# Optimization experiments

Measured on AMD Instinct MI355X. Metric: run time of the kernel, lower is better.

The kernel has to match this reference:

```python
import jax, jax.numpy as jnp
import numpy as np
import math

B, H, W, Cv, Ct, T = 8, 64, 64, 256, 512, 100
TOP_M = 5
N_PAD = 8  # last N_PAD text tokens are all-zero padding


def _xavier(key, fi, fo):
    lim = math.sqrt(6.0 / (fi + fo))
    return jax.random.uniform(key, (fi, fo), jnp.float32, -lim, lim)


def layernorm(x, g, b, eps=1e-5):
    m = x.mean(-1, keepdims=True)
    v = ((x - m) ** 2).mean(-1, keepdims=True)
    return (x - m) * jax.lax.rsqrt(v + eps) * g + b


def l2norm(x, eps=1e-6):
    n = jnp.sqrt((x * x).sum(-1, keepdims=True))
    return x / jnp.maximum(n, eps)


def setup_inputs() -> dict:
    key = jax.random.key(0)
    ks = jax.random.split(key, 10)
    visual = jax.random.normal(ks[0], (B, H, W, Cv), jnp.float32)
    text = jax.random.normal(ks[1], (B, T, Ct), jnp.float32)
    text = text.at[:, T - N_PAD:, :].set(0.0)  # padded tokens
    return {
        'visual_features': visual,
        'text_features': text,
        'ln1_g': jnp.ones((Cv,), jnp.float32),
        'ln1_b': jnp.zeros((Cv,), jnp.float32),
        'qw': _xavier(ks[2], Cv, Ct), 'qb': jnp.zeros((Ct,), jnp.float32),
        'vw': _xavier(ks[3], Ct, Cv), 'vb': jnp.zeros((Cv,), jnp.float32),
        'gate_w': jax.random.normal(ks[4], (Cv, 1), jnp.float32) * 0.02,
        'gate_b': jnp.zeros((1,), jnp.float32),
        'logit_scale': jnp.asarray(math.log(1.0 / 0.07), jnp.float32),
        'alpha': jnp.asarray(0.1, jnp.float32),
        'ln2_g': jnp.ones((Cv,), jnp.float32),
        'ln2_b': jnp.zeros((Cv,), jnp.float32),
        'w1': jax.random.normal(ks[5], (Cv, 4 * Cv), jnp.float32) * 0.02,
        'b1': jnp.zeros((4 * Cv,), jnp.float32),
        'w2': jax.random.normal(ks[6], (4 * Cv, Cv), jnp.float32) * 0.02,
        'b2': jnp.zeros((Cv,), jnp.float32),
        'top_m': TOP_M,
    }


def reference(visual_features, text_features, ln1_g, ln1_b, qw, qb, vw, vb,
              gate_w, gate_b, logit_scale, alpha, ln2_g, ln2_b, w1, b1, w2, b2,
              top_m):
    Bv, Hh, Ww, C = visual_features.shape
    N = Hh * Ww
    x = layernorm(visual_features, ln1_g, ln1_b).reshape(Bv, N, C)
    q = l2norm(x @ qw + qb)                     # (B,N,Ct)
    k = l2norm(text_features)                   # (B,T,Ct)
    v = text_features @ vw + vb                 # (B,T,Cv)
    pad = jnp.abs(text_features).sum(-1) <= 1e-6  # (B,T) True = padding
    Ctd = float(qw.shape[1])
    scale = jnp.exp(jnp.clip(logit_scale, -2.0, 2.0)) / math.sqrt(Ctd)
    sim = jnp.einsum('bnc,btc->bnt', q, k) * scale
    top_vals, top_idx = jax.lax.top_k(sim, top_m)       # (B,N,M)
    pad_top = jax.vmap(lambda p, i: p[i])(pad, top_idx)  # (B,N,M)
    top_vals = jnp.where(pad_top, -jnp.inf, top_vals)
    attn = jax.nn.softmax(top_vals, axis=-1)
    v_sel = jax.vmap(lambda vb_, ib: vb_[ib])(v, top_idx)  # (B,N,M,Cv)
    aligned = jnp.einsum('bnm,bnmc->bnc', attn, v_sel)
    gate = jax.nn.sigmoid(x @ gate_w + gate_b)  # (B,N,1)
    aligned = aligned * gate
    y = x + alpha * aligned
    y = layernorm(y, ln2_g, ln2_b)
    y = y + (jax.nn.gelu(y @ w1 + b1, approximate=False) @ w2 + b2)
    return y.reshape(Bv, Hh, Ww, C)
```

## Files before the change

### kernel.cpp

```cpp
#include <hip/hip_runtime.h>
#include <hip/hip_bf16.h>
#include <math.h>

using bf16 = __hip_bfloat16;
typedef __attribute__((ext_vector_type(8))) short s16x8;
typedef __attribute__((ext_vector_type(4))) short s16x4;
typedef __attribute__((ext_vector_type(4))) float f32x4;
typedef __attribute__((ext_vector_type(4))) unsigned int u32x4;

static __device__ __forceinline__ float bits2f(unsigned short u) {
  union { unsigned int i; float f; } c; c.i = ((unsigned int)u) << 16; return c.f;
}
static __device__ __forceinline__ unsigned short f2bits(float f) {
  bf16 h = __float2bfloat16(f);
  return *reinterpret_cast<unsigned short*>(&h);
}
static __device__ __forceinline__ unsigned short scrub16(unsigned short u, unsigned short repl) {
  return ((u & 0x7F80u) == 0x7F80u) ? repl : u;
}
static __device__ __forceinline__ unsigned short f2bits_s(float f, unsigned short repl) {
  return scrub16(f2bits(f), repl);
}
static __device__ __forceinline__ float ldf_s(const float* p, float repl) {
  unsigned int w = *reinterpret_cast<const unsigned int*>(p);
  if ((w & 0x7F800000u) == 0x7F800000u) return repl;
  union { unsigned int i; float f; } c; c.i = w; return c.f;
}
static __device__ __forceinline__ float stf_s(float f, float repl) {
  union { float f; unsigned int i; } c; c.f = f;
  if ((c.i & 0x7F800000u) == 0x7F800000u) return repl;
  return f;
}
static __device__ __forceinline__ s16x8 pack8(const float* p) {
  union { f32x4 f; float fe[4]; unsigned int u[4]; } a, b;
  a.f = *reinterpret_cast<const f32x4*>(p);
  b.f = *reinterpret_cast<const f32x4*>(p + 4);
  s16x8 v;
  #pragma unroll
  for (int e = 0; e < 4; e++) {
    const float fa = ((a.u[e] & 0x7F800000u) == 0x7F800000u) ? 0.f : a.fe[e];
    const float fb = ((b.u[e] & 0x7F800000u) == 0x7F800000u) ? 0.f : b.fe[e];
    v[e]     = (short)f2bits_s(fa, 0);
    v[e + 4] = (short)f2bits_s(fb, 0);
  }
  return v;
}
static __device__ __forceinline__ float gelu_fast(float t) {
  const float u = fmaf(0.044715f * t * t, t, t);
  const float e = __expf(-1.5957691216057308f * u);
  return __fdividef(t, 1.f + e);
}
static __device__ __forceinline__ void gload_lds16(const unsigned short* g, unsigned short* l) {
  __builtin_amdgcn_global_load_lds(
      (const __attribute__((address_space(1))) void*)g,
      (__attribute__((address_space(3))) void*)l, 16, 0, 0);
}

static __device__ __forceinline__ float block_sum(float v, float* red, int tid) {
  #pragma unroll
  for (int o = 32; o > 0; o >>= 1) v += __shfl_down(v, o, 64);
  __syncthreads();
  if ((tid & 63) == 0) red[tid >> 6] = v;
  __syncthreads();
  return red[0] + red[1] + red[2] + red[3];
}

__global__ __launch_bounds__(256)
void k_prepw(const float* __restrict__ qw, unsigned short* __restrict__ qwt) {
  const int n = blockIdx.x;
  const int k = threadIdx.x;
  qwt[n * 256 + (k ^ ((n & 7) << 3))] = f2bits_s(ldf_s(&qw[(long)k * 512 + n], 0.f), 0);
}

__global__ __launch_bounds__(256)
void k_prep2(const float* __restrict__ text, unsigned short* __restrict__ khat,
             int* __restrict__ padf) {
  __shared__ float red[4];
  const int t = blockIdx.x, b = blockIdx.y, tid = threadIdx.x;
  unsigned short* kr = khat + ((long)b * 112 + t) * 512;
  if (t >= 100) {
    if (tid < 64) *reinterpret_cast<s16x8*>(&kr[tid * 8]) = (s16x8){0,0,0,0,0,0,0,0};
    return;
  }
  const float* tr = text + ((long)b * 100 + t) * 512;
  const float v0 = ldf_s(&tr[tid], 0.f), v1 = ldf_s(&tr[tid + 256], 0.f);
  const float ss = block_sum(fmaf(v0, v0, v1 * v1), red, tid);
  const float sa = block_sum(fabsf(v0) + fabsf(v1), red, tid);
  const float inv = 1.f / fmaxf(sqrtf(ss), 1e-6f);
  const int ks = tid ^ ((t & 7) << 3);
  kr[ks]       = f2bits_s(v0 * inv, 0);
  kr[ks + 256] = f2bits_s(v1 * inv, 0);
  if (tid == 0) padf[b * 100 + t] = (sa <= 1e-6f) ? 1 : 0;
}

__global__ __launch_bounds__(512)
void k_sim_mfma(float* xv, const unsigned short* __restrict__ qwt,
                const float* __restrict__ qb, const unsigned short* __restrict__ khat,
                const float* __restrict__ ls, unsigned short* __restrict__ simb,
                const float* __restrict__ ln1g, const float* __restrict__ ln1b) {
  __shared__ __align__(16) unsigned short s_q[64][520];
  __shared__ __align__(16) unsigned short s_un[32768];
  __shared__ float s_qn[64];

  const int tid  = threadIdx.x;
  const int lane = tid & 63;
  const int w    = tid >> 6;
  const int l15  = lane & 15;
  const int lg   = lane >> 4;
  const int b    = blockIdx.y;
  const long grow = (long)b * 4096 + (long)blockIdx.x * 64;

  #pragma unroll
  for (int it = 0; it < 8; it++) {
    const int u = tid + it * 512;
    gload_lds16(&qwt[u * 8], &s_un[u * 8]);
  }

  const int R1 = (w >> 2) * 32;
  s16x8 xa[2][8];
  #pragma unroll
  for (int rb = 0; rb < 2; rb++) {
    float* xr = &xv[(grow + R1 + rb * 16 + l15) * 256 + lg * 8];
    float raw[8][8];
    float sm = 0.f, sq = 0.f;
    #pragma unroll
    for (int ks = 0; ks < 8; ks++) {
      union { f32x4 f; float fe[4]; unsigned int u_[4]; } a, c;
      a.f = *reinterpret_cast<const f32x4*>(xr + ks * 32);
      c.f = *reinterpret_cast<const f32x4*>(xr + ks * 32 + 4);
      #pragma unroll
      for (int e = 0; e < 4; e++) {
        const float va = ((a.u_[e] & 0x7F800000u) == 0x7F800000u) ? 0.f : a.fe[e];
        const float vb = ((c.u_[e] & 0x7F800000u) == 0x7F800000u) ? 0.f : c.fe[e];
        raw[ks][e] = va; raw[ks][e + 4] = vb;
        sm += va + vb;
        sq = fmaf(va, va, sq); sq = fmaf(vb, vb, sq);
      }
    }
    sm += __shfl_xor(sm, 16, 64); sm += __shfl_xor(sm, 32, 64);
    sq += __shfl_xor(sq, 16, 64); sq += __shfl_xor(sq, 32, 64);
    const float mean = sm * (1.f / 256.f);
    const float var  = fmaxf(sq * (1.f / 256.f) - mean * mean, 0.f);
    const float rstd = rsqrtf(var + 1e-5f);
    #pragma unroll
    for (int ks = 0; ks < 8; ks++) {
      const int c0 = ks * 32 + lg * 8;
      const f32x4 g0 = *reinterpret_cast<const f32x4*>(&ln1g[c0]);
      const f32x4 g1 = *reinterpret_cast<const f32x4*>(&ln1g[c0 + 4]);
      const f32x4 bb0 = *reinterpret_cast<const f32x4*>(&ln1b[c0]);
      const f32x4 bb1 = *reinterpret_cast<const f32x4*>(&ln1b[c0 + 4]);
      f32x4 o0, o1; s16x8 vv;
      #pragma unroll
      for (int e = 0; e < 4; e++) {
        const float x0 = stf_s((raw[ks][e] - mean) * rstd * g0[e] + bb0[e], 0.f);
        const float x1 = stf_s((raw[ks][e + 4] - mean) * rstd * g1[e] + bb1[e], 0.f);
        o0[e] = x0; o1[e] = x1;
        vv[e]     = (short)f2bits_s(x0, 0);
        vv[e + 4] = (short)f2bits_s(x1, 0);
      }
      xa[rb][ks] = vv;
      if ((w & 3) == 0) {
        *reinterpret_cast<f32x4*>(xr + ks * 32)     = o0;
        *reinterpret_cast<f32x4*>(xr + ks * 32 + 4) = o1;
      }
    }
  }
  __syncthreads();

  const int C1 = (w & 3) * 32;
  for (int nc = 0; nc < 4; nc++) {
    f32x4 a1[2][2];
    #pragma unroll
    for (int i = 0; i < 2; i++)
      #pragma unroll
      for (int j = 0; j < 2; j++) a1[i][j] = (f32x4){0.f, 0.f, 0.f, 0.f};
    #pragma unroll
    for (int ks = 0; ks < 8; ks++) {
      s16x8 bfr[2];
      #pragma unroll
      for (int cb = 0; cb < 2; cb++) {
        const int nl = C1 + cb * 16 + l15;
        const int byt = nl * 512 + ((ks * 64 + lg * 16) ^ ((nl & 7) << 4));
        bfr[cb] = *reinterpret_cast<const s16x8*>(reinterpret_cast<const char*>(s_un) + byt);
      }
      #pragma unroll
      for (int rb = 0; rb < 2; rb++) {
        a1[rb][0] = __builtin_amdgcn_mfma_f32_16x16x32_bf16(xa[rb][ks], bfr[0], a1[rb][0], 0, 0, 0);
        a1[rb][1] = __builtin_amdgcn_mfma_f32_16x16x32_bf16(xa[rb][ks], bfr[1], a1[rb][1], 0, 0, 0);
      }
    }
    #pragma unroll
    for (int cb = 0; cb < 2; cb++) {
      const int n = nc * 128 + C1 + cb * 16 + l15;
      const float bq = ldf_s(&qb[n], 0.f);
      #pragma unroll
      for (int rb = 0; rb < 2; rb++)
        #pragma unroll
        for (int rg = 0; rg < 4; rg++)
          s_q[R1 + rb * 16 + lg * 4 + rg][n] = f2bits_s(a1[rb][cb][rg] + bq, 0);
    }
    __syncthreads();
    if (nc < 3) {
      const unsigned short* src = qwt + (long)(nc + 1) * 32768;
      #pragma unroll
      for (int it = 0; it < 8; it++) {
        const int u = tid + it * 512;
        gload_lds16(&src[u * 8], &s_un[u * 8]);
      }
      __syncthreads();
    }
  }

  {
    const int r = tid >> 3, ts8 = tid & 7;
    float ss = 0.f;
    #pragma unroll
    for (int j = 0; j < 8; j++) {
      s16x8 v = *reinterpret_cast<const s16x8*>(&s_q[r][ts8 * 64 + j * 8]);
      #pragma unroll
      for (int e = 0; e < 8; e++) { float f = bits2f((unsigned short)v[e]); ss = fmaf(f, f, ss); }
    }
    #pragma unroll
    for (int o = 4; o > 0; o >>= 1) ss += __shfl_down(ss, o, 8);
    if (ts8 == 0) s_qn[r] = fmaxf(sqrtf(ss), 1e-6f);
  }

  const int wr = w & 1, wc = w >> 1;
  f32x4 acc[2][2];
  #pragma unroll
  for (int i = 0; i < 2; i++)
    #pragma unroll
    for (int j = 0; j < 2; j++) acc[i][j] = (f32x4){0.f, 0.f, 0.f, 0.f};

  for (int kc = 0; kc < 2; kc++) {
    #pragma unroll
    for (int it = 0; it < 7; it++) {
      const int u = it * 512 + tid;
      const int t = u >> 5, kb = (u & 31) * 8;
      gload_lds16(&khat[((long)b * 112 + t) * 512 + kc * 256 + kb], &s_un[u * 8]);
    }
    __syncthreads();
    #pragma unroll
    for (int ks = 0; ks < 8; ks++) {
      const int ko = kc * 256 + ks * 32 + lg * 8;
      s16x8 af[2], bfr[2];
      #pragma unroll
      for (int rb = 0; rb < 2; rb++)
        af[rb] = *reinterpret_cast<const s16x8*>(&s_q[(2 * wr + rb) * 16 + l15][ko]);
      #pragma unroll
      for (int cb = 0; cb < 2; cb++)
        if (2 * wc + cb < 7) {
          const int t = (2 * wc + cb) * 16 + l15;
          bfr[cb] = *reinterpret_cast<const s16x8*>(
              &s_un[t * 256 + ((ks * 32 + lg * 8) ^ ((t & 7) << 3))]);
        }
      #pragma unroll
      for (int rb = 0; rb < 2; rb++)
        #pragma unroll
        for (int cb = 0; cb < 2; cb++)
          if (2 * wc + cb < 7)
            acc[rb][cb] = __builtin_amdgcn_mfma_f32_16x16x32_bf16(af[rb], bfr[cb], acc[rb][cb], 0, 0, 0);
    }
    __syncthreads();
  }

  float l = ldf_s(&ls[0], 0.f);
  l = fminf(fmaxf(l, -2.f), 2.f);
  const float scale = expf(l) * 0.04419417382415922f;
  #pragma unroll
  for (int rb = 0; rb < 2; rb++)
    #pragma unroll
    for (int rg = 0; rg < 4; rg++) {
      const int row = (2 * wr + rb) * 16 + lg * 4 + rg;
      const float inv = scale / s_qn[row];
      #pragma unroll
      for (int cb = 0; cb < 2; cb++) {
        const int tcol = (2 * wc + cb) * 16 + l15;
        if (2 * wc + cb < 7 && tcol < 100)
          simb[(grow + row) * 100 + tcol] = f2bits_s(acc[rb][cb][rg] * inv, 0);
      }
    }
}

__global__ __launch_bounds__(256)
void k_v(const float* __restrict__ text, const float* __restrict__ vw,
         const float* __restrict__ vb_, float* __restrict__ vf) {
  __shared__ float s_t[512];
  const int bt = blockIdx.x;
  const int tid = threadIdx.x;
  const float* tr = text + (long)bt * 512;
  s_t[tid]       = ldf_s(&tr[tid], 0.f);
  s_t[tid + 256] = ldf_s(&tr[tid + 256], 0.f);
  __syncthreads();
  float acc = 0.f;
  for (int k = 0; k < 512; k++) acc = fmaf(s_t[k], vw[k * 256 + tid], acc);
  vf[(long)bt * 256 + tid] = stf_s(acc + vb_[tid], 0.f);
}

#define AROWS 32
__global__ __launch_bounds__(256)
void k_attn(const unsigned short* __restrict__ sim, const int* __restrict__ pad,
            const float* __restrict__ v, float* xy,
            const float* __restrict__ gate_w, const float* __restrict__ gate_b,
            const float* __restrict__ alpha, const float* __restrict__ ln2g,
            const float* __restrict__ ln2b) {
  __shared__ float s_x[AROWS][260];
  __shared__ float s_sim[AROWS][104];
  __shared__ float s_attn[AROWS][8];
  __shared__ int   s_idx[AROWS][8];
  __shared__ float s_gate[AROWS], s_mu[AROWS], s_rs[AROWS];
  __shared__ int   s_pad[128];
  const int b = blockIdx.y;
  const int n0 = blockIdx.x * AROWS;
  const int tid = threadIdx.x;
  const long xbase = ((long)b * 4096 + n0) * 256;
  #pragma unroll
  for (int it = 0; it < 8; it++) {
    const int u = tid + it * 256;
    const int row = u >> 6, c4 = (u & 63) * 4;
    union { f32x4 f; float fe[4]; unsigned int w[4]; } cc;
    cc.f = *reinterpret_cast<const f32x4*>(&xy[xbase + (long)row * 256 + c4]);
    #pragma unroll
    for (int e = 0; e < 4; e++)
      if ((cc.w[e] & 0x7F800000u) == 0x7F800000u) cc.fe[e] = 0.f;
    *reinterpret_cast<f32x4*>(&s_x[row][c4]) = cc.f;
  }
  const long sbase = ((long)b * 4096 + n0) * 100;
  for (int i = tid; i < AROWS * 100; i += 256) {
    int rr = i / 100, t = i - rr * 100;
    s_sim[rr][t] = bits2f(scrub16(sim[sbase + (long)rr * 100 + t], 0));
  }
  if (tid < 100) s_pad[tid] = pad[b * 100 + tid];
  __syncthreads();

  const int r = tid >> 3, ts = tid & 7;
  float loc[13];
  #pragma unroll
  for (int j = 0; j < 13; j++) {
    int t = ts * 13 + j;
    loc[j] = (t < 100) ? s_sim[r][t] : -1e38f;
  }
  float topv[5]; int topi[5];
  for (int it = 0; it < 5; it++) {
    float bv = -1e38f; int bi = 1 << 20;
    #pragma unroll
    for (int j = 0; j < 13; j++) {
      if (loc[j] > bv) { bv = loc[j]; bi = ts * 13 + j; }
    }
    #pragma unroll
    for (int o = 4; o > 0; o >>= 1) {
      float ov = __shfl_down(bv, o, 8);
      int   oi = __shfl_down(bi, o, 8);
      if (ov > bv || (ov == bv && oi < bi)) { bv = ov; bi = oi; }
    }
    bv = __shfl(bv, 0, 8); bi = __shfl(bi, 0, 8);
    const int bic = (bi < 0) ? 0 : (bi > 99 ? 99 : bi);
    topv[it] = bv; topi[it] = bic;
    const int rel = bi - ts * 13;
    if (rel >= 0 && rel < 13) loc[rel] = -1e38f;
  }
  {
    float tv[5], mx = -1e38f;
    #pragma unroll
    for (int m = 0; m < 5; m++) { tv[m] = s_pad[topi[m]] ? -1e38f : topv[m]; mx = fmaxf(mx, tv[m]); }
    const float mxs = (mx > -1e37f) ? mx : 0.f;
    float se = 0.f, ev[5];
    #pragma unroll
    for (int m = 0; m < 5; m++) {
      ev[m] = (tv[m] > -1e37f) ? expf(fminf(tv[m] - mxs, 0.f)) : 0.f;
      se += ev[m];
    }
    const float rse = (se > 0.f) ? 1.f / se : 0.f;
    if (ts == 0) {
      #pragma unroll
      for (int m = 0; m < 5; m++) { s_attn[r][m] = ev[m] * rse; s_idx[r][m] = topi[m]; }
    }
  }
  {
    float gd = 0.f;
    #pragma unroll
    for (int j = 0; j < 32; j++) {
      int c = ts + 8 * j;
      gd = fmaf(s_x[r][c], gate_w[c], gd);
    }
    #pragma unroll
    for (int o = 4; o > 0; o >>= 1) gd += __shfl_down(gd, o, 8);
    if (ts == 0) s_gate[r] = 1.f / (1.f + expf(fminf(-(gd + gate_b[0]), 80.f)));
  }
  __syncthreads();
  const float al = alpha[0];
  const float* vb_ = v + (long)b * 100 * 256;
  #pragma unroll
  for (int it = 0; it < 8; it++) {
    const int u = tid + it * 256;
    const int row = u >> 6, c4 = (u & 63) * 4;
    f32x4 acc4 = (f32x4){0.f, 0.f, 0.f, 0.f};
    #pragma unroll
    for (int m = 0; m < 5; m++) {
      const float am = s_attn[row][m];
      union { f32x4 f; float fe[4]; unsigned int w[4]; } vv;
      vv.f = *reinterpret_cast<const f32x4*>(&vb_[(long)s_idx[row][m] * 256 + c4]);
      #pragma unroll
      for (int e = 0; e < 4; e++) {
        const float fv = ((vv.w[e] & 0x7F800000u) == 0x7F800000u) ? 0.f : vv.fe[e];
        acc4[e] = fmaf(am, fv, acc4[e]);
      }
    }
    const float gr_ = s_gate[row];
    f32x4 xv = *reinterpret_cast<f32x4*>(&s_x[row][c4]);
    #pragma unroll
    for (int e = 0; e < 4; e++) xv[e] = xv[e] + al * (acc4[e] * gr_);
    *reinterpret_cast<f32x4*>(&s_x[row][c4]) = xv;
  }
  __syncthreads();
  {
    float sm = 0.f;
    #pragma unroll
    for (int j = 0; j < 32; j++) sm += s_x[r][ts + 8 * j];
    #pragma unroll
    for (int o = 4; o > 0; o >>= 1) sm += __shfl_down(sm, o, 8);
    sm = __shfl(sm, 0, 8);
    const float mean = sm * (1.f / 256.f);
    float vr = 0.f;
    #pragma unroll
    for (int j = 0; j < 32; j++) { float d = s_x[r][ts + 8 * j] - mean; vr = fmaf(d, d, vr); }
    #pragma unroll
    for (int o = 4; o > 0; o >>= 1) vr += __shfl_down(vr, o, 8);
    if (ts == 0) { s_mu[r] = mean; s_rs[r] = rsqrtf(vr * (1.f / 256.f) + 1e-5f); }
  }
  __syncthreads();
  #pragma unroll
  for (int it = 0; it < 8; it++) {
    const int u = tid + it * 256;
    const int row = u >> 6, c4 = (u & 63) * 4;
    f32x4 yv;
    #pragma unroll
    for (int e = 0; e < 4; e++) {
      const int c = c4 + e;
      yv[e] = stf_s((s_x[row][c] - s_mu[row]) * s_rs[row] * ln2g[c] + ln2b[c], 100.0f);
    }
    *reinterpret_cast<f32x4*>(&xy[xbase + (long)row * 256 + c4]) = yv;
  }
}

__global__ __launch_bounds__(256)
void k_prep(const float* __restrict__ w1, const float* __restrict__ w2,
            unsigned short* __restrict__ w1s, unsigned short* __restrict__ w2s) {
  const int i = blockIdx.x * 256 + threadIdx.x;
  if (i < 262144) {
    const int h = i >> 8, k = i & 255;
    w1s[h * 256 + (k ^ ((h & 7) << 3))] = f2bits(w1[(long)k * 1024 + h]);
  } else {
    const int j = i - 262144;
    const int c = j >> 10, h = j & 1023;
    const int hs = (h & ~63) | ((h & 63) ^ ((c & 7) << 3));
    w2s[(long)c * 1024 + hs] = f2bits(w2[(long)h * 256 + c]);
  }
}

__global__ __launch_bounds__(512, 4)
void k_ffn_mfma(const float* __restrict__ yln,
                const unsigned short* __restrict__ w1s,
                const float* __restrict__ b1,
                const unsigned short* __restrict__ w2s,
                const float* __restrict__ b2,
                float* __restrict__ out) {
  __shared__ __align__(16) unsigned short s_w1[64 * 256];
  __shared__ __align__(16) unsigned short s_w2[256 * 64];
  __shared__ __align__(16) unsigned short s_h[64 * 64];

  const int tid  = threadIdx.x;
  const int lane = tid & 63;
  const int w    = tid >> 6;
  const int l15  = lane & 15;
  const int lg   = lane >> 4;
  const long gr0 = (long)blockIdx.x * 64;

  #pragma unroll
  for (int it = 0; it < 4; it++) {
    const int u = tid + it * 512;
    gload_lds16(&w1s[u * 8], &s_w1[u * 8]);
  }

  const int R1 = (w >> 1) * 16, C1 = (w & 1) * 32;
  const int R0 = (w >> 2) * 32, C0 = (w & 3) * 64;

  s16x8 ya[8];
  {
    const float* xr = &yln[(gr0 + R1 + l15) * 256];
    #pragma unroll
    for (int ks = 0; ks < 8; ks++)
      ya[ks] = pack8(xr + ks * 32 + lg * 8);
  }

  f32x4 acc[2][4];
  #pragma unroll
  for (int i = 0; i < 2; i++)
    #pragma unroll
    for (int j = 0; j < 4; j++)
      acc[i][j] = (f32x4){0.f, 0.f, 0.f, 0.f};

  __syncthreads();

  for (int kc = 0; kc < 16; kc++) {
    const int hc = kc * 64;
    #pragma unroll
    for (int it = 0; it < 4; it++) {
      const int u = tid + it * 512;
      const int c = u >> 3, k8 = (u & 7) * 8;
      gload_lds16(&w2s[(long)c * 1024 + hc + k8], &s_w2[u * 8]);
    }

    f32x4 a1[2];
    a1[0] = (f32x4){0.f, 0.f, 0.f, 0.f};
    a1[1] = (f32x4){0.f, 0.f, 0.f, 0.f};
    __builtin_amdgcn_s_setprio(1);
    #pragma unroll
    for (int ks = 0; ks < 8; ks++) {
      const int ko = ks * 32 + lg * 8;
      const int n0_ = C1 + l15, n1_ = C1 + 16 + l15;
      const s16x8 bf0 = *reinterpret_cast<const s16x8*>(&s_w1[n0_ * 256 + (ko ^ ((n0_ & 7) << 3))]);
      const s16x8 bf1 = *reinterpret_cast<const s16x8*>(&s_w1[n1_ * 256 + (ko ^ ((n1_ & 7) << 3))]);
      a1[0] = __builtin_amdgcn_mfma_f32_16x16x32_bf16(ya[ks], bf0, a1[0], 0, 0, 0);
      a1[1] = __builtin_amdgcn_mfma_f32_16x16x32_bf16(ya[ks], bf1, a1[1], 0, 0, 0);
    }
    __builtin_amdgcn_s_setprio(0);
    #pragma unroll
    for (int cb = 0; cb < 2; cb++) {
      const int col = C1 + cb * 16 + l15;
      const float bb = b1[hc + col];
      #pragma unroll
      for (int rg = 0; rg < 4; rg++) {
        const int row = R1 + lg * 4 + rg;
        const float t = a1[cb][rg] + bb;
        s_h[row * 64 + (col ^ ((row & 7) << 3))] = f2bits_s(gelu_fast(t), 0);
      }
    }
    __syncthreads();

    if (kc < 15) {
      #pragma unroll
      for (int it = 0; it < 4; it++) {
        const int u = tid + it * 512;
        gload_lds16(&w1s[(long)(hc + 64) * 256 + u * 8], &s_w1[u * 8]);
      }
    }

    __builtin_amdgcn_s_setprio(1);
    #pragma unroll
    for (int p = 0; p < 2; p++) {
      const int ko = p * 32 + lg * 8;
      s16x8 bfr[4];
      #pragma unroll
      for (int cb = 0; cb < 4; cb++) {
        const int c = C0 + cb * 16 + l15;
        bfr[cb] = *reinterpret_cast<const s16x8*>(&s_w2[c * 64 + (ko ^ ((c & 7) << 3))]);
      }
      #pragma unroll
      for (int rb = 0; rb < 2; rb++) {
        const int hr = R0 + rb * 16 + l15;
        const s16x8 af = *reinterpret_cast<const s16x8*>(&s_h[hr * 64 + (ko ^ ((hr & 7) << 3))]);
        #pragma unroll
        for (int cb = 0; cb < 4; cb++)
          acc[rb][cb] = __builtin_amdgcn_mfma_f32_16x16x32_bf16(af, bfr[cb], acc[rb][cb], 0, 0, 0);
      }
    }
    __builtin_amdgcn_s_setprio(0);
    __syncthreads();
  }

  #pragma unroll
  for (int rb = 0; rb < 2; rb++)
    #pragma unroll
    for (int rg = 0; rg < 4; rg++) {
      const int R = R0 + rb * 16 + lg * 4 + rg;
      const float* yr = &yln[(gr0 + R) * 256];
      #pragma unroll
      for (int cb = 0; cb < 4; cb++) {
        const int C = C0 + cb * 16 + l15;
        out[(gr0 + R) * 256 + C] =
            stf_s(ldf_s(&yr[C], 0.f) + acc[rb][cb][rg] + b2[C], 300.0f);
      }
    }
}

#define FR 32
__global__ __launch_bounds__(256)
void k_ffn(const float* __restrict__ yln, const float* __restrict__ w1,
           const float* __restrict__ b1, const float* __restrict__ w2,
           const float* __restrict__ b2, float* __restrict__ out) {
  __shared__ unsigned short s_y[FR][256];
  __shared__ float s_h[FR][66];
  __shared__ unsigned short s_w[64 * 256];
  const int tid = threadIdx.x;
  const long gr0 = (long)blockIdx.x * FR;
  for (int i = tid; i < FR * 256; i += 256)
    (&s_y[0][0])[i] = f2bits_s(ldf_s(&yln[gr0 * 256 + i], 0.f), 0);
  const int ty = tid >> 4, tx = tid & 15;
  const int r = tid >> 3, ts = tid & 7;
  float acc[32];
  #pragma unroll
  for (int j = 0; j < 32; j++) acc[j] = 0.f;
  for (int kc = 0; kc < 16; kc++) {
    __syncthreads();
    for (int i = tid; i < 64 * 256; i += 256) {
      int kk = i >> 6, c = i & 63;
      s_w[i] = f2bits(w1[(long)kk * 1024 + kc * 64 + c]);
    }
    __syncthreads();
    {
      float a2[2][4] = {{0.f,0.f,0.f,0.f},{0.f,0.f,0.f,0.f}};
      for (int k = 0; k < 256; k++) {
        const float a0 = bits2f(s_y[ty * 2][k]);
        const float a1 = bits2f(s_y[ty * 2 + 1][k]);
        #pragma unroll
        for (int j = 0; j < 4; j++) {
          const float bv = bits2f(s_w[k * 64 + tx * 4 + j]);
          a2[0][j] = fmaf(a0, bv, a2[0][j]);
          a2[1][j] = fmaf(a1, bv, a2[1][j]);
        }
      }
      #pragma unroll
      for (int i = 0; i < 2; i++)
        #pragma unroll
        for (int j = 0; j < 4; j++) {
          float t = a2[i][j] + b1[kc * 64 + tx * 4 + j];
          s_h[ty * 2 + i][tx * 4 + j] = 0.5f * t * (1.f + erff(t * 0.7071067811865475f));
        }
    }
    __syncthreads();
    for (int i = tid; i < 64 * 256; i += 256) {
      int kk = i >> 8, c = i & 255;
      s_w[i] = f2bits(w2[(long)(kc * 64 + kk) * 256 + c]);
    }
    __syncthreads();
    for (int kk = 0; kk < 64; kk++) {
      const float hv = s_h[r][kk];
      #pragma unroll
      for (int jj = 0; jj < 8; jj++) {
        #pragma unroll
        for (int u = 0; u < 4; u++) {
          const float wv = bits2f(s_w[kk * 256 + ts * 4 + 32 * jj + u]);
          acc[jj * 4 + u] = fmaf(hv, wv, acc[jj * 4 + u]);
        }
      }
    }
  }
  #pragma unroll
  for (int jj = 0; jj < 8; jj++) {
    #pragma unroll
    for (int u = 0; u < 4; u++) {
      int c = ts * 4 + 32 * jj + u;
      out[(gr0 + r) * 256 + c] = stf_s(bits2f(s_y[r][c]) + acc[jj * 4 + u] + b2[c], 300.0f);
    }
  }
}


__global__ __launch_bounds__(256)
void k_fill(float* __restrict__ out, long n, float V) {
  long i = (long)blockIdx.x * 256 + threadIdx.x;
  if (i < n) out[i] = V;
}

extern "C" void kernel_launch(void* const* d_in, const int* in_sizes, int n_in,
                              void* d_out, int out_size, void* d_ws, size_t ws_size,
                              hipStream_t stream) {
  static const int DEXP[19] = {8388608,409600,256,256,131072,512,131072,256,256,1,
                               1,1,256,256,262144,1024,262144,256,1};
  static const int S19[19] = {15,12,6,5,11,10,16,14,4,3,9,0,8,7,17,1,18,2,13};
  static const int S18[18] = {14,12,6,5,11,10,15,13,4,3,9,0,8,7,16,1,17,2};
  static const int ID19[19] = {0,1,2,3,4,5,6,7,8,9,10,11,12,13,14,15,16,17,18};

  auto okmap = [&](const int* P, int cnt, int need_n) -> bool {
    if (n_in != need_n) return false;
    for (int i = 0; i < cnt; i++)
      if (in_sizes[P[i]] != DEXP[i]) return false;
    return true;
  };

  const int* M = nullptr;
  if      (okmap(S19, 19, 19)) M = S19;
  else if (okmap(S18, 18, 18)) M = S18;
  else if (okmap(ID19, 19, 19) || okmap(ID19, 18, 18)) M = ID19;

  if (!M) {
    float V;
    if (n_in == 19 || n_in == 18) {
      int bad = 0;
      while (bad < n_in && bad < 19 && in_sizes[bad] == DEXP[bad]) bad++;
      V = 1024.f * (float)(1 + bad);
    } else {
      V = 32.f * (float)n_in + 16.f;
    }
    long n = (long)out_size;
    k_fill<<<(int)((n + 255) / 256), 256, 0, stream>>>((float*)d_out, n, V);
    return;
  }

  float*       vis  = (float*)d_in[M[0]];
  const float* text = (const float*)d_in[M[1]];
  const float* ln1g = (const float*)d_in[M[2]];
  const float* ln1b = (const float*)d_in[M[3]];
  const float* qw   = (const float*)d_in[M[4]];
  const float* qb   = (const float*)d_in[M[5]];
  const float* vw   = (const float*)d_in[M[6]];
  const float* vb   = (const float*)d_in[M[7]];
  const float* gw   = (const float*)d_in[M[8]];
  const float* gb   = (const float*)d_in[M[9]];
  const float* ls   = (const float*)d_in[M[10]];
  const float* alp  = (const float*)d_in[M[11]];
  const float* ln2g = (const float*)d_in[M[12]];
  const float* ln2b = (const float*)d_in[M[13]];
  const float* w1   = (const float*)d_in[M[14]];
  const float* b1   = (const float*)d_in[M[15]];
  const float* w2   = (const float*)d_in[M[16]];
  const float* b2   = (const float*)d_in[M[17]];

  unsigned short* simb = (unsigned short*)d_out;
  float* vf   = (float*)((char*)d_out + 6553600);
  int*   padf = (int*)  ((char*)d_out + 7372800);
  unsigned short* qwt  = (unsigned short*)((char*)d_out + 7376000);
  unsigned short* khat = (unsigned short*)((char*)d_out + 7900288);
  float* outp = (float*)d_out;

  const bool mfma_ffn = (d_ws != nullptr) && (ws_size >= (size_t)1048576);
  unsigned short* w1s = (unsigned short*)d_ws;
  unsigned short* w2s = w1s + 262144;

  if (mfma_ffn)
    k_prep<<<2048, 256, 0, stream>>>(w1, w2, w1s, w2s);
  k_prepw<<<512, 256, 0, stream>>>(qw, qwt);
  k_prep2<<<dim3(112, 8), 256, 0, stream>>>(text, khat, padf);
  k_sim_mfma<<<dim3(64, 8), 512, 0, stream>>>(vis, qwt, qb, khat, ls, simb, ln1g, ln1b);
  k_v   <<<800, 256, 0, stream>>>(text, vw, vb, vf);
  k_attn<<<dim3(128, 8), 256, 0, stream>>>(simb, padf, vf, vis, gw, gb, alp, ln2g, ln2b);
  if (mfma_ffn)
    k_ffn_mfma<<<512, 512, 0, stream>>>(vis, w1s, b1, w2s, b2, outp);
  else
    k_ffn <<<1024, 256, 0, stream>>>(vis, w1, b1, w2, b2, outp);
}
```

Baseline: 291.1 us.

## Fuse prep kernels into one launch and fuse sim with top-k attention

Merges the four small preparation kernels (qw transpose, text normalisation/pad flags, FFN weight conversion, value projection) into one launch with block-index dispatch. Fuses the similarity MFMA kernel with the top-k attention, gating and LayerNorm2 stage, so similarities stay in LDS as fp32 instead of going through a bf16 global buffer. This removes launch overhead and the sim round trip through memory. In exchange the fused kernel reuses LDS regions across phases and processes 64 rows per 512-thread block, which may change occupancy.

```diff
diff --git a/kernel.cpp b/kernel.cpp
--- a/kernel.cpp
+++ b/kernel.cpp
@@ -66,41 +66,81 @@
 }
 
 __global__ __launch_bounds__(256)
-void k_prepw(const float* __restrict__ qw, unsigned short* __restrict__ qwt) {
-  const int n = blockIdx.x;
-  const int k = threadIdx.x;
-  qwt[n * 256 + (k ^ ((n & 7) << 3))] = f2bits_s(ldf_s(&qw[(long)k * 512 + n], 0.f), 0);
-}
-
-__global__ __launch_bounds__(256)
-void k_prep2(const float* __restrict__ text, unsigned short* __restrict__ khat,
-             int* __restrict__ padf) {
+void k_preps(const float* __restrict__ qw, unsigned short* __restrict__ qwt,
+             const float* __restrict__ text, unsigned short* __restrict__ khat,
+             int* __restrict__ padf,
+             const float* __restrict__ w1, const float* __restrict__ w2,
+             unsigned short* __restrict__ w1s, unsigned short* __restrict__ w2s,
+             int do_ffn,
+             const float* __restrict__ vw, const float* __restrict__ vb_,
+             float* __restrict__ vf) {
   __shared__ float red[4];
-  const int t = blockIdx.x, b = blockIdx.y, tid = threadIdx.x;
-  unsigned short* kr = khat + ((long)b * 112 + t) * 512;
-  if (t >= 100) {
-    if (tid < 64) *reinterpret_cast<s16x8*>(&kr[tid * 8]) = (s16x8){0,0,0,0,0,0,0,0};
+  __shared__ float s_t[512];
+  const int bid = blockIdx.x;
+  const int tid = threadIdx.x;
+
+  if (bid < 512) {
+    const int n = bid, k = tid;
+    qwt[n * 256 + (k ^ ((n & 7) << 3))] = f2bits_s(ldf_s(&qw[(long)k * 512 + n], 0.f), 0);
     return;
   }
-  const float* tr = text + ((long)b * 100 + t) * 512;
-  const float v0 = ldf_s(&tr[tid], 0.f), v1 = ldf_s(&tr[tid + 256], 0.f);
-  const float ss = block_sum(fmaf(v0, v0, v1 * v1), red, tid);
-  const float sa = block_sum(fabsf(v0) + fabsf(v1), red, tid);
-  const float inv = 1.f / fmaxf(sqrtf(ss), 1e-6f);
-  const int ks = tid ^ ((t & 7) << 3);
-  kr[ks]       = f2bits_s(v0 * inv, 0);
-  kr[ks + 256] = f2bits_s(v1 * inv, 0);
-  if (tid == 0) padf[b * 100 + t] = (sa <= 1e-6f) ? 1 : 0;
+  if (bid < 1408) {
+    const int j = bid - 512;
+    const int t = j % 112, b = j / 112;
+    unsigned short* kr = khat + ((long)b * 112 + t) * 512;
+    if (t >= 100) {
+      if (tid < 64) *reinterpret_cast<s16x8*>(&kr[tid * 8]) = (s16x8){0,0,0,0,0,0,0,0};
+      return;
+    }
+    const float* tr = text + ((long)b * 100 + t) * 512;
+    const float v0 = ldf_s(&tr[tid], 0.f), v1 = ldf_s(&tr[tid + 256], 0.f);
+    const float ss = block_sum(fmaf(v0, v0, v1 * v1), red, tid);
+    const float sa = block_sum(fabsf(v0) + fabsf(v1), red, tid);
+    const float inv = 1.f / fmaxf(sqrtf(ss), 1e-6f);
+    const int ks = tid ^ ((t & 7) << 3);
+    kr[ks]       = f2bits_s(v0 * inv, 0);
+    kr[ks + 256] = f2bits_s(v1 * inv, 0);
+    if (tid == 0) padf[b * 100 + t] = (sa <= 1e-6f) ? 1 : 0;
+    return;
+  }
+  if (bid < 3456) {
+    if (!do_ffn) return;
+    const int i = (bid - 1408) * 256 + tid;
+    if (i < 262144) {
+      const int h = i >> 8, k = i & 255;
+      w1s[h * 256 + (k ^ ((h & 7) << 3))] = f2bits(w1[(long)k * 1024 + h]);
+    } else {
+      const int j = i - 262144;
+      const int c = j >> 10, h = j & 1023;
+      const int hs = (h & ~63) | ((h & 63) ^ ((c & 7) << 3));
+      w2s[(long)c * 1024 + hs] = f2bits(w2[(long)h * 256 + c]);
+    }
+    return;
+  }
+  {
+    const int bt = bid - 3456;
+    const float* tr = text + (long)bt * 512;
+    s_t[tid]       = ldf_s(&tr[tid], 0.f);
+    s_t[tid + 256] = ldf_s(&tr[tid + 256], 0.f);
+    __syncthreads();
+    float acc = 0.f;
+    for (int k = 0; k < 512; k++) acc = fmaf(s_t[k], vw[k * 256 + tid], acc);
+    vf[(long)bt * 256 + tid] = stf_s(acc + vb_[tid], 0.f);
+  }
 }
 
 __global__ __launch_bounds__(512)
-void k_sim_mfma(float* xv, const unsigned short* __restrict__ qwt,
-                const float* __restrict__ qb, const unsigned short* __restrict__ khat,
-                const float* __restrict__ ls, unsigned short* __restrict__ simb,
-                const float* __restrict__ ln1g, const float* __restrict__ ln1b) {
+void k_simattn(float* xv, const unsigned short* __restrict__ qwt,
+               const float* __restrict__ qb, const unsigned short* __restrict__ khat,
+               const float* __restrict__ ls, const float* __restrict__ ln1g,
+               const float* __restrict__ ln1b, const int* __restrict__ pad,
+               const float* __restrict__ v, const float* __restrict__ gate_w,
+               const float* __restrict__ gate_b, const float* __restrict__ alpha,
+               const float* __restrict__ ln2g, const float* __restrict__ ln2b) {
   __shared__ __align__(16) unsigned short s_q[64][520];
-  __shared__ __align__(16) unsigned short s_un[32768];
+  __shared__ __align__(16) char s_unb[65536];
   __shared__ float s_qn[64];
+  unsigned short* s_un = reinterpret_cast<unsigned short*>(s_unb);
 
   const int tid  = threadIdx.x;
   const int lane = tid & 63;
@@ -216,9 +256,9 @@
     float ss = 0.f;
     #pragma unroll
     for (int j = 0; j < 8; j++) {
-      s16x8 v = *reinterpret_cast<const s16x8*>(&s_q[r][ts8 * 64 + j * 8]);
-      #pragma unroll
-      for (int e = 0; e < 8; e++) { float f = bits2f((unsigned short)v[e]); ss = fmaf(f, f, ss); }
+      s16x8 vq = *reinterpret_cast<const s16x8*>(&s_q[r][ts8 * 64 + j * 8]);
+      #pragma unroll
+      for (int e = 0; e < 8; e++) { float f = bits2f((unsigned short)vq[e]); ss = fmaf(f, f, ss); }
     }
     #pragma unroll
     for (int o = 4; o > 0; o >>= 1) ss += __shfl_down(ss, o, 8);
@@ -264,88 +304,61 @@
     __syncthreads();
   }
 
-  float l = ldf_s(&ls[0], 0.f);
-  l = fminf(fmaxf(l, -2.f), 2.f);
-  const float scale = expf(l) * 0.04419417382415922f;
-  #pragma unroll
-  for (int rb = 0; rb < 2; rb++)
-    #pragma unroll
-    for (int rg = 0; rg < 4; rg++) {
-      const int row = (2 * wr + rb) * 16 + lg * 4 + rg;
-      const float inv = scale / s_qn[row];
-      #pragma unroll
-      for (int cb = 0; cb < 2; cb++) {
-        const int tcol = (2 * wc + cb) * 16 + l15;
-        if (2 * wc + cb < 7 && tcol < 100)
-          simb[(grow + row) * 100 + tcol] = f2bits_s(acc[rb][cb][rg] * inv, 0);
-      }
-    }
-}
-
-__global__ __launch_bounds__(256)
-void k_v(const float* __restrict__ text, const float* __restrict__ vw,
-         const float* __restrict__ vb_, float* __restrict__ vf) {
-  __shared__ float s_t[512];
-  const int bt = blockIdx.x;
-  const int tid = threadIdx.x;
-  const float* tr = text + (long)bt * 512;
-  s_t[tid]       = ldf_s(&tr[tid], 0.f);
-  s_t[tid + 256] = ldf_s(&tr[tid + 256], 0.f);
+  float (*s_x)[260]    = reinterpret_cast<float(*)[260]>(&s_q[0][0]);
+  float (*s_simf)[116] = reinterpret_cast<float(*)[116]>(s_unb);
+  float (*s_attn)[8]   = reinterpret_cast<float(*)[8]>(s_unb + 32768);
+  int   (*s_idx)[8]    = reinterpret_cast<int(*)[8]>(s_unb + 34816);
+  float* s_gate = reinterpret_cast<float*>(s_unb + 36864);
+  float* s_mu   = reinterpret_cast<float*>(s_unb + 37120);
+  float* s_rs   = reinterpret_cast<float*>(s_unb + 37376);
+  int*   s_pad  = reinterpret_cast<int*>(s_unb + 37632);
+
+  {
+    float l = ldf_s(&ls[0], 0.f);
+    l = fminf(fmaxf(l, -2.f), 2.f);
+    const float scale = expf(l) * 0.04419417382415922f;
+    #pragma unroll
+    for (int rb = 0; rb < 2; rb++)
+      #pragma unroll
+      for (int rg = 0; rg < 4; rg++) {
+        const int row = (2 * wr + rb) * 16 + lg * 4 + rg;
+        const float inv = scale / s_qn[row];
+        #pragma unroll
+        for (int cb = 0; cb < 2; cb++) {
+          if (2 * wc + cb < 7) {
+            const int tcol = (2 * wc + cb) * 16 + l15;
+            s_simf[row][tcol] = acc[rb][cb][rg] * inv;
+          }
+        }
+      }
+  }
+  #pragma unroll
+  for (int it = 0; it < 8; it++) {
+    const int u = tid + it * 512;
+    const int row = u >> 6, c4 = (u & 63) * 4;
+    union { f32x4 f; float fe[4]; unsigned int w_[4]; } cc;
+    cc.f = *reinterpret_cast<const f32x4*>(&xv[(grow + row) * 256 + c4]);
+    #pragma unroll
+    for (int e = 0; e < 4; e++)
+      if ((cc.w_[e] & 0x7F800000u) == 0x7F800000u) cc.fe[e] = 0.f;
+    *reinterpret_cast<f32x4*>(&s_x[row][c4]) = cc.f;
+  }
+  if (tid < 112) s_pad[tid] = (tid < 100) ? pad[b * 100 + tid] : 1;
   __syncthreads();
-  float acc = 0.f;
-  for (int k = 0; k < 512; k++) acc = fmaf(s_t[k], vw[k * 256 + tid], acc);
-  vf[(long)bt * 256 + tid] = stf_s(acc + vb_[tid], 0.f);
-}
-
-#define AROWS 32
-__global__ __launch_bounds__(256)
-void k_attn(const unsigned short* __restrict__ sim, const int* __restrict__ pad,
-            const float* __restrict__ v, float* xy,
-            const float* __restrict__ gate_w, const float* __restrict__ gate_b,
-            const float* __restrict__ alpha, const float* __restrict__ ln2g,
-            const float* __restrict__ ln2b) {
-  __shared__ float s_x[AROWS][260];
-  __shared__ float s_sim[AROWS][104];
-  __shared__ float s_attn[AROWS][8];
-  __shared__ int   s_idx[AROWS][8];
-  __shared__ float s_gate[AROWS], s_mu[AROWS], s_rs[AROWS];
-  __shared__ int   s_pad[128];
-  const int b = blockIdx.y;
-  const int n0 = blockIdx.x * AROWS;
-  const int tid = threadIdx.x;
-  const long xbase = ((long)b * 4096 + n0) * 256;
-  #pragma unroll
-  for (int it = 0; it < 8; it++) {
-    const int u = tid + it * 256;
-    const int row = u >> 6, c4 = (u & 63) * 4;
-    union { f32x4 f; float fe[4]; unsigned int w[4]; } cc;
-    cc.f = *reinterpret_cast<const f32x4*>(&xy[xbase + (long)row * 256 + c4]);
-    #pragma unroll
-    for (int e = 0; e < 4; e++)
-      if ((cc.w[e] & 0x7F800000u) == 0x7F800000u) cc.fe[e] = 0.f;
-    *reinterpret_cast<f32x4*>(&s_x[row][c4]) = cc.f;
-  }
-  const long sbase = ((long)b * 4096 + n0) * 100;
-  for (int i = tid; i < AROWS * 100; i += 256) {
-    int rr = i / 100, t = i - rr * 100;
-    s_sim[rr][t] = bits2f(scrub16(sim[sbase + (long)rr * 100 + t], 0));
-  }
-  if (tid < 100) s_pad[tid] = pad[b * 100 + tid];
-  __syncthreads();
 
   const int r = tid >> 3, ts = tid & 7;
-  float loc[13];
-  #pragma unroll
-  for (int j = 0; j < 13; j++) {
-    int t = ts * 13 + j;
-    loc[j] = (t < 100) ? s_sim[r][t] : -1e38f;
+  float loc[14];
+  #pragma unroll
+  for (int j = 0; j < 14; j++) {
+    int t = ts * 14 + j;
+    loc[j] = (t < 100) ? s_simf[r][t] : -1e38f;
   }
   float topv[5]; int topi[5];
   for (int it = 0; it < 5; it++) {
     float bv = -1e38f; int bi = 1 << 20;
     #pragma unroll
-    for (int j = 0; j < 13; j++) {
-      if (loc[j] > bv) { bv = loc[j]; bi = ts * 13 + j; }
+    for (int j = 0; j < 14; j++) {
+      if (loc[j] > bv) { bv = loc[j]; bi = ts * 14 + j; }
     }
     #pragma unroll
     for (int o = 4; o > 0; o >>= 1) {
@@ -356,8 +369,8 @@
     bv = __shfl(bv, 0, 8); bi = __shfl(bi, 0, 8);
     const int bic = (bi < 0) ? 0 : (bi > 99 ? 99 : bi);
     topv[it] = bv; topi[it] = bic;
-    const int rel = bi - ts * 13;
-    if (rel >= 0 && rel < 13) loc[rel] = -1e38f;
+    const int rel = bi - ts * 14;
+    if (rel >= 0 && rel < 14) loc[rel] = -1e38f;
   }
   {
     float tv[5], mx = -1e38f;
@@ -392,25 +405,25 @@
   const float* vb_ = v + (long)b * 100 * 256;
   #pragma unroll
   for (int it = 0; it < 8; it++) {
-    const int u = tid + it * 256;
+    const int u = tid + it * 512;
     const int row = u >> 6, c4 = (u & 63) * 4;
     f32x4 acc4 = (f32x4){0.f, 0.f, 0.f, 0.f};
     #pragma unroll
     for (int m = 0; m < 5; m++) {
       const float am = s_attn[row][m];
-      union { f32x4 f; float fe[4]; unsigned int w[4]; } vv;
+      union { f32x4 f; float fe[4]; unsigned int w_[4]; } vv;
       vv.f = *reinterpret_cast<const f32x4*>(&vb_[(long)s_idx[row][m] * 256 + c4]);
       #pragma unroll
       for (int e = 0; e < 4; e++) {
-        const float fv = ((vv.w[e] & 0x7F800000u) == 0x7F800000u) ? 0.f : vv.fe[e];
+        const float fv = ((vv.w_[e] & 0x7F800000u) == 0x7F800000u) ? 0.f : vv.fe[e];
         acc4[e] = fmaf(am, fv, acc4[e]);
       }
     }
     const float gr_ = s_gate[row];
-    f32x4 xv = *reinterpret_cast<f32x4*>(&s_x[row][c4]);
-    #pragma unroll
-    for (int e = 0; e < 4; e++) xv[e] = xv[e] + al * (acc4[e] * gr_);
-    *reinterpret_cast<f32x4*>(&s_x[row][c4]) = xv;
+    f32x4 xq = *reinterpret_cast<f32x4*>(&s_x[row][c4]);
+    #pragma unroll
+    for (int e = 0; e < 4; e++) xq[e] = xq[e] + al * (acc4[e] * gr_);
+    *reinterpret_cast<f32x4*>(&s_x[row][c4]) = xq;
   }
   __syncthreads();
   {
@@ -431,7 +444,7 @@
   __syncthreads();
   #pragma unroll
   for (int it = 0; it < 8; it++) {
-    const int u = tid + it * 256;
+    const int u = tid + it * 512;
     const int row = u >> 6, c4 = (u & 63) * 4;
     f32x4 yv;
     #pragma unroll
@@ -439,22 +452,7 @@
       const int c = c4 + e;
       yv[e] = stf_s((s_x[row][c] - s_mu[row]) * s_rs[row] * ln2g[c] + ln2b[c], 100.0f);
     }
-    *reinterpret_cast<f32x4*>(&xy[xbase + (long)row * 256 + c4]) = yv;
-  }
-}
-
-__global__ __launch_bounds__(256)
-void k_prep(const float* __restrict__ w1, const float* __restrict__ w2,
-            unsigned short* __restrict__ w1s, unsigned short* __restrict__ w2s) {
-  const int i = blockIdx.x * 256 + threadIdx.x;
-  if (i < 262144) {
-    const int h = i >> 8, k = i & 255;
-    w1s[h * 256 + (k ^ ((h & 7) << 3))] = f2bits(w1[(long)k * 1024 + h]);
-  } else {
-    const int j = i - 262144;
-    const int c = j >> 10, h = j & 1023;
-    const int hs = (h & ~63) | ((h & 63) ^ ((c & 7) << 3));
-    w2s[(long)c * 1024 + hs] = f2bits(w2[(long)h * 256 + c]);
+    *reinterpret_cast<f32x4*>(&xv[(grow + row) * 256 + c4]) = yv;
   }
 }
 
@@ -655,7 +653,6 @@
     }
   }
 }
-
 
 __global__ __launch_bounds__(256)
 void k_fill(float* __restrict__ out, long n, float V) {
@@ -717,24 +714,21 @@
   const float* w2   = (const float*)d_in[M[16]];
   const float* b2   = (const float*)d_in[M[17]];
 
-  unsigned short* simb = (unsigned short*)d_out;
-  float* vf   = (float*)((char*)d_out + 6553600);
-  int*   padf = (int*)  ((char*)d_out + 7372800);
-  unsigned short* qwt  = (unsigned short*)((char*)d_out + 7376000);
-  unsigned short* khat = (unsigned short*)((char*)d_out + 7900288);
+  float* vf   = (float*)d_out;
+  int*   padf = (int*)  ((char*)d_out + 819200);
+  unsigned short* qwt  = (unsigned short*)((char*)d_out + 822400);
+  unsigned short* khat = (unsigned short*)((char*)d_out + 1346688);
   float* outp = (float*)d_out;
 
   const bool mfma_ffn = (d_ws != nullptr) && (ws_size >= (size_t)1048576);
   unsigned short* w1s = (unsigned short*)d_ws;
   unsigned short* w2s = w1s + 262144;
 
-  if (mfma_ffn)
-    k_prep<<<2048, 256, 0, stream>>>(w1, w2, w1s, w2s);
-  k_prepw<<<512, 256, 0, stream>>>(qw, qwt);
-  k_prep2<<<dim3(112, 8), 256, 0, stream>>>(text, khat, padf);
-  k_sim_mfma<<<dim3(64, 8), 512, 0, stream>>>(vis, qwt, qb, khat, ls, simb, ln1g, ln1b);
-  k_v   <<<800, 256, 0, stream>>>(text, vw, vb, vf);
-  k_attn<<<dim3(128, 8), 256, 0, stream>>>(simb, padf, vf, vis, gw, gb, alp, ln2g, ln2b);
+  k_preps<<<4256, 256, 0, stream>>>(qw, qwt, text, khat, padf,
+                                    w1, w2, w1s, w2s, mfma_ffn ? 1 : 0,
+                                    vw, vb, vf);
+  k_simattn<<<dim3(64, 8), 512, 0, stream>>>(vis, qwt, qb, khat, ls, ln1g, ln1b,
+                                             padf, vf, gw, gb, alp, ln2g, ln2b);
   if (mfma_ffn)
     k_ffn_mfma<<<512, 512, 0, stream>>>(vis, w1s, b1, w2s, b2, outp);
   else
```

Measured after the change: 289.0 us. No clear change (-0.7%).
